# Performance work log

Hardware: AMD Instinct MI355X
Metric: run time of the kernel (lower is better)

## Reference

```python
import jax, jax.numpy as jnp
import numpy as np
from jax import lax

B, T, C, H, W = 4, 10, 96, 32, 32
L = 13
OUT = 96


def _conv(x, w, b, pad):
    y = lax.conv_general_dilated(x, w, (1, 1), [(pad, pad), (pad, pad)],
                                 dimension_numbers=('NCHW', 'OIHW', 'NCHW'))
    return y + b[None, :, None, None]


def _leaky(x):
    return jnp.where(x >= 0, x, 0.2 * x)  # LeakyReLU(0.2)


def _bilinear_warp(img, gx, gy):
    # img (B,C,H,W); gx,gy (B,L,H,W) absolute pixel coords; zero padding outside.
    # Equivalent to torch grid_sample(bilinear, zeros, align_corners=True) as used in HKO wrap().
    def per_b(im, gxb, gyb):
        h, w = im.shape[1], im.shape[2]
        x0 = jnp.floor(gxb)
        y0 = jnp.floor(gyb)
        wx = (gxb - x0)[None]  # (1,L,H,W)
        wy = (gyb - y0)[None]

        def g(xi, yi):
            valid = (xi >= 0) & (xi <= w - 1) & (yi >= 0) & (yi <= h - 1)
            xc = jnp.clip(xi, 0, w - 1).astype(jnp.int32)
            yc = jnp.clip(yi, 0, h - 1).astype(jnp.int32)
            return im[:, yc, xc] * valid[None].astype(im.dtype)  # (C,L,H,W)

        v00 = g(x0, y0)
        v01 = g(x0 + 1, y0)
        v10 = g(x0, y0 + 1)
        v11 = g(x0 + 1, y0 + 1)
        out = (v00 * (1 - wx) + v01 * wx) * (1 - wy) + (v10 * (1 - wx) + v11 * wx) * wy
        return out.transpose(1, 0, 2, 3)  # (L,C,H,W)

    return jax.vmap(per_b)(img, gx, gy)  # (B,L,C,H,W)


def setup_inputs() -> dict:
    key = jax.random.key(0)
    ks = jax.random.split(key, 8)
    s = 0.05
    return {
        "x": jax.random.normal(ks[0], (B, T, C, H, W), jnp.float32),
        "h0": jnp.zeros((B, C, H, W), jnp.float32),
        "i2h_w": jax.random.normal(ks[1], (3 * C, C, 3, 3), jnp.float32) * s,
        "i2h_b": jnp.zeros((3 * C,), jnp.float32),
        "i2f_w": jax.random.normal(ks[2], (32, C, 5, 5), jnp.float32) * s,
        "i2f_b": jnp.zeros((32,), jnp.float32),
        "h2f_w": jax.random.normal(ks[3], (32, C, 5, 5), jnp.float32) * s,
        "h2f_b": jnp.zeros((32,), jnp.float32),
        "flow_w": jax.random.normal(ks[4], (2 * L, 32, 5, 5), jnp.float32) * s,
        "flow_b": jnp.zeros((2 * L,), jnp.float32),
        "ret_w": jax.random.normal(ks[5], (3 * C, L * C, 1, 1), jnp.float32) * s,
        "ret_b": jnp.zeros((3 * C,), jnp.float32),
        "ct_w": jax.random.normal(ks[6], (C * T, OUT * T, 4, 4), jnp.float32) * s,  # torch ConvTranspose2d layout (in,out,kh,kw)
        "ct_b": jnp.zeros((OUT * T,), jnp.float32),
    }


def reference(x, h0, i2h_w, i2h_b, i2f_w, i2f_b, h2f_w, h2f_b,
              flow_w, flow_b, ret_w, ret_b, ct_w, ct_b):
    xs = x.transpose(1, 0, 2, 3, 4)  # (T,B,C,H,W)
    flat = xs.reshape(T * B, C, H, W)
    i2h_all = _conv(flat, i2h_w, i2h_b, 1).reshape(T, B, 3 * C, H, W)
    i2f_all = _conv(flat, i2f_w, i2f_b, 2).reshape(T, B, 32, H, W)
    yy, xx = jnp.meshgrid(jnp.arange(H, dtype=x.dtype),
                          jnp.arange(W, dtype=x.dtype), indexing='ij')

    def step(h, inp):
        i2h_t, i2f_t = inp
        f = _leaky(i2f_t + _conv(h, h2f_w, h2f_b, 2))
        flows = _conv(f, flow_w, flow_b, 2).reshape(B, L, 2, H, W)
        # HKO: wrap(prev_h, -flow) -> sample at grid - flow
        gx = xx - flows[:, :, 0]  # (B,L,H,W)
        gy = yy - flows[:, :, 1]
        warped = _bilinear_warp(h, gx, gy).reshape(B, L * C, H, W)
        h2h = _conv(warped, ret_w, ret_b, 0)  # 1x1 ret conv
        ir, iu, im_ = jnp.split(i2h_t, 3, axis=1)
        hr, hu, hm = jnp.split(h2h, 3, axis=1)
        r = jax.nn.sigmoid(ir + hr)
        u = jax.nn.sigmoid(iu + hu)
        new_mem = _leaky(im_ + r * hm)
        h_next = u * h + (1.0 - u) * new_mem
        return h_next, h_next

    _, ys = lax.scan(step, h0, (i2h_all, i2f_all))  # (T,B,C,H,W)
    y = ys.transpose(1, 0, 2, 3, 4).reshape(B, T * C, H, W)
    # ConvTranspose2d(k=4, s=2, p=1) == conv(flipped kernel, lhs_dilation=2, pad=k-1-p=2)
    wt = jnp.flip(ct_w, (2, 3)).transpose(1, 0, 2, 3)  # (out,in,kh,kw)
    y = lax.conv_general_dilated(y, wt, (1, 1), [(2, 2), (2, 2)],
                                 lhs_dilation=(2, 2),
                                 dimension_numbers=('NCHW', 'OIHW', 'NCHW'))
    y = _leaky(y + ct_b[None, :, None, None])
    return y.reshape(B, T, OUT, 2 * H, 2 * W)
```

## Files before the change

### kernel.cpp

```cpp
#include <hip/hip_runtime.h>
#include <math.h>
#include <stddef.h>

#define B_  4
#define T_  10
#define C_  96
#define H_  32
#define W_  32
#define HW_ 1024
#define L_  13
#define OUT_ 96

typedef __attribute__((ext_vector_type(4))) float f32x4;
typedef __attribute__((ext_vector_type(8))) short bf16x8;

__device__ __forceinline__ float leaky_f(float v) { return v >= 0.f ? v : 0.2f * v; }
__device__ __forceinline__ float sigmoid_f(float v) { return 1.f / (1.f + expf(-v)); }
__device__ __forceinline__ unsigned short f2bf(float f) {
    unsigned u = __float_as_uint(f);
    return (unsigned short)((u + 0x7FFFu + ((u >> 16) & 1u)) >> 16);
}
__device__ __forceinline__ float bf2f(unsigned short s) {
    return __uint_as_float((unsigned)s << 16);
}
__device__ __forceinline__ void gload_lds16(const void* g, void* l) {
    __builtin_amdgcn_global_load_lds(
        (const __attribute__((address_space(1))) unsigned int*)g,
        (__attribute__((address_space(3))) unsigned int*)l, 16, 0, 0);
}

__global__ __launch_bounds__(256) void conv5x5_x_k(
    const float* __restrict__ x, const float* __restrict__ w,
    const float* __restrict__ bias, float* __restrict__ out)
{
    const int px  = threadIdx.x & 63;
    const int g   = threadIdx.x >> 6;
    const int row = px >> 5, col = px & 31;
    const int y0  = blockIdx.x * 2;
    const int oc0 = blockIdx.y * 8 + g * 2;
    const int n   = blockIdx.z;
    const int b   = n % B_;
    const int t   = n / B_;
    const float* xin = x + ((size_t)(b * T_ + t) * C_) * HW_;

    __shared__ float tile[6][36];
    float acc0 = 0.f, acc1 = 0.f;

    for (int c = 0; c < C_; ++c) {
        const float* xc = xin + (size_t)c * HW_;
        if (threadIdx.x < 216) {
            int r = threadIdx.x / 36, cc = threadIdx.x % 36;
            int yy = y0 + r - 2, xx = cc - 2;
            tile[r][cc] = (yy >= 0 && yy < 32 && xx >= 0 && xx < 32) ? xc[yy * 32 + xx] : 0.f;
        }
        __syncthreads();
        const float* w0 = w + ((size_t)oc0 * C_ + c) * 25;
        const float* w1 = w0 + (size_t)C_ * 25;
        #pragma unroll
        for (int dy = 0; dy < 5; ++dy)
            #pragma unroll
            for (int dx = 0; dx < 5; ++dx) {
                float v = tile[row + dy][col + dx];
                acc0 = fmaf(v, w0[dy * 5 + dx], acc0);
                acc1 = fmaf(v, w1[dy * 5 + dx], acc1);
            }
        __syncthreads();
    }
    const int hw = (y0 + row) * 32 + col;
    out[((size_t)n * 32 + oc0) * HW_ + hw]     = acc0 + bias[oc0];
    out[((size_t)n * 32 + oc0 + 1) * HW_ + hw] = acc1 + bias[oc0 + 1];
}

__global__ __launch_bounds__(256) void conv5x5_k(
    const float* __restrict__ in, int in_bstr, int cin, int cout,
    const float* __restrict__ w, const float* __restrict__ bias,
    const float* __restrict__ addsrc, int do_leaky,
    float* __restrict__ out)
{
    const int px  = threadIdx.x & 63;
    const int g   = threadIdx.x >> 6;
    const int row = px >> 5, col = px & 31;
    const int y0  = blockIdx.x * 2;
    const int oc0 = blockIdx.y * 8 + g * 2;
    const int b   = blockIdx.z;
    const int ocw0 = min(oc0, cout - 1);
    const int ocw1 = min(oc0 + 1, cout - 1);

    __shared__ float tile[6][36];
    float acc0 = 0.f, acc1 = 0.f;

    for (int c = 0; c < cin; ++c) {
        const float* xc = in + ((size_t)b * in_bstr + c) * HW_;
        if (threadIdx.x < 216) {
            int r = threadIdx.x / 36, cc = threadIdx.x % 36;
            int yy = y0 + r - 2, xx = cc - 2;
            tile[r][cc] = (yy >= 0 && yy < 32 && xx >= 0 && xx < 32) ? xc[yy * 32 + xx] : 0.f;
        }
        __syncthreads();
        const float* w0 = w + ((size_t)ocw0 * cin + c) * 25;
        const float* w1 = w + ((size_t)ocw1 * cin + c) * 25;
        #pragma unroll
        for (int dy = 0; dy < 5; ++dy)
            #pragma unroll
            for (int dx = 0; dx < 5; ++dx) {
                float v = tile[row + dy][col + dx];
                acc0 = fmaf(v, w0[dy * 5 + dx], acc0);
                acc1 = fmaf(v, w1[dy * 5 + dx], acc1);
            }
        __syncthreads();
    }
    const int hw = (y0 + row) * 32 + col;
    if (oc0 < cout) {
        float r = acc0 + bias[oc0];
        if (addsrc) r += addsrc[((size_t)b * cout + oc0) * HW_ + hw];
        if (do_leaky) r = leaky_f(r);
        out[((size_t)b * cout + oc0) * HW_ + hw] = r;
    }
    if (oc0 + 1 < cout) {
        float r = acc1 + bias[oc0 + 1];
        if (addsrc) r += addsrc[((size_t)b * cout + oc0 + 1) * HW_ + hw];
        if (do_leaky) r = leaky_f(r);
        out[((size_t)b * cout + oc0 + 1) * HW_ + hw] = r;
    }
}

__global__ __launch_bounds__(256) void warp_k(
    const float* __restrict__ h, const float* __restrict__ flows,
    unsigned short* __restrict__ warped_s)
{
    const int hw = (blockIdx.x << 6) + (threadIdx.x & 63);
    const int cg = threadIdx.x >> 6;
    const int l  = blockIdx.y;
    const int b  = blockIdx.z;
    const int py = hw >> 5, px = hw & 31;

    const float fx = flows[((size_t)b * (2 * L_) + 2 * l) * HW_ + hw];
    const float fy = flows[((size_t)b * (2 * L_) + 2 * l + 1) * HW_ + hw];
    const float gx = (float)px - fx;
    const float gy = (float)py - fy;
    const float x0f = floorf(gx), y0f = floorf(gy);
    const float wx = gx - x0f, wy = gy - y0f;
    const int x0 = (int)x0f, y0 = (int)y0f;
    const int x1 = x0 + 1, y1 = y0 + 1;

    const bool vx0 = (x0 >= 0 && x0 <= 31), vx1 = (x1 >= 0 && x1 <= 31);
    const bool vy0 = (y0 >= 0 && y0 <= 31), vy1 = (y1 >= 0 && y1 <= 31);
    const int xc0 = min(max(x0, 0), 31), xc1 = min(max(x1, 0), 31);
    const int yc0 = min(max(y0, 0), 31), yc1 = min(max(y1, 0), 31);
    const int o00 = yc0 * 32 + xc0, o01 = yc0 * 32 + xc1;
    const int o10 = yc1 * 32 + xc0, o11 = yc1 * 32 + xc1;
    const float w00 = (vx0 && vy0) ? (1.f - wx) * (1.f - wy) : 0.f;
    const float w01 = (vx1 && vy0) ? wx * (1.f - wy) : 0.f;
    const float w10 = (vx0 && vy1) ? (1.f - wx) * wy : 0.f;
    const float w11 = (vx1 && vy1) ? wx * wy : 0.f;

    const float* hb = h + ((size_t)b * C_ + cg * 24) * HW_;
    unsigned short* ob = warped_s + ((size_t)b * 2496 + 2 * (l * C_ + cg * 24)) * HW_ + hw;
    for (int cc = 0; cc < 24; ++cc) {
        const float* hc = hb + (size_t)cc * HW_;
        float v = hc[o00] * w00 + hc[o01] * w01 + hc[o10] * w10 + hc[o11] * w11;
        unsigned short hi = f2bf(v);
        ob[(size_t)(2 * cc) * HW_]     = hi;
        ob[(size_t)(2 * cc + 1) * HW_] = f2bf(v - bf2f(hi));
    }
}

__global__ __launch_bounds__(256) void wxprep_k(
    const float* __restrict__ i2h_w, unsigned short* __restrict__ WxS)
{
    const int idx = blockIdx.x * 256 + threadIdx.x;
    const int m = idx / 2624, kp = idx - m * 2624;
    unsigned short r = 0;
    if (m < 288) {
        if (kp < 1728) {
            const int k = kp >> 1;
            const int d = k / 96, c = k - d * 96;
            r = f2bf(i2h_w[((size_t)m * 96 + c) * 9 + d]);
        } else if (kp < 2592) {
            const int k = kp - 1728;
            const int d = k / 96, c = k - d * 96;
            const float w = i2h_w[((size_t)m * 96 + c) * 9 + d];
            const unsigned short hi = f2bf(w);
            r = f2bf(w - bf2f(hi));
        }
    }
    WxS[idx] = r;
}

__global__ __launch_bounds__(256) void wrprep_k(
    const float* __restrict__ ret_w, unsigned short* __restrict__ WrS)
{
    const int idx = blockIdx.x * 256 + threadIdx.x;
    const int m = idx / 3840, kp = idx - m * 3840;
    unsigned short r = 0;
    if (m < 288) {
        if (kp < 2496) {
            r = f2bf(ret_w[(size_t)m * 1248 + (kp >> 1)]);
        } else if (kp < 3744) {
            const float w = ret_w[(size_t)m * 1248 + (kp - 2496)];
            const unsigned short hi = f2bf(w);
            r = f2bf(w - bf2f(hi));
        }
    }
    WrS[idx] = r;
}

__global__ __launch_bounds__(256) void wprep_k(
    const float* __restrict__ ct_w, unsigned short* __restrict__ Wp)
{
    const int idx = blockIdx.x * 256 + threadIdx.x;
    const int ic  = idx % 960;
    const int oc  = (idx / 960) & 1023;
    const int p   = idx / (960 * 1024);
    const int ry  = p >> 1, rx = p & 1;

    unsigned long long pack = 0ull;
    if (oc < 960) {
        #pragma unroll
        for (int a = 0; a < 2; ++a)
            #pragma unroll
            for (int e = 0; e < 2; ++e) {
                const int ky = 3 - 2 * a - ry, kx = 3 - 2 * e - rx;
                float f = ct_w[(((size_t)ic * 960 + oc) * 4 + ky) * 4 + kx];
                pack |= (unsigned long long)f2bf(f) << ((a * 2 + e) * 16);
            }
    }
    *(unsigned long long*)(Wp + ((size_t)(p * 1024 + oc) * 3840 + ic * 4)) = pack;
}

__global__ __launch_bounds__(256) void i2h_gemm_k(
    const float* __restrict__ x, const unsigned short* __restrict__ WxS,
    const float* __restrict__ bias, float* __restrict__ out)
{
    __shared__ unsigned short sA[8192];
    __shared__ unsigned short sB[8192];

    const int t    = threadIdx.x;
    const int lane = t & 63;
    const int wave = t >> 6;
    const int wr   = wave >> 1, wc = wave & 1;
    const int l15  = lane & 15, l4 = lane >> 4;

    const int px0 = blockIdx.x * 128;
    const int m0  = blockIdx.y * 128;

    const unsigned short* aPtr[4];
    int aOff[4];
    #pragma unroll
    for (int i = 0; i < 4; ++i) {
        const int lin = i * 256 + t;
        const int r = lin >> 3;
        const int c = (lin & 7) ^ (r & 7);
        aPtr[i] = WxS + (size_t)(m0 + r) * 2624 + c * 8;
        aOff[i] = lin * 8;
    }

    const int jr    = t & 127;
    const int cbase = t >> 7;
    const int pos   = px0 + jr;
    const int img   = pos >> 10;
    const int hw    = pos & 1023;
    const int ycell = hw >> 5, xcell = hw & 31;
    const int bb = img % B_, tt = img / B_;
    const float* xb = x + ((size_t)(bb * T_ + tt) * C_) * HW_;
    unsigned short* ldsB = sB + jr * 64;

    int offA[4][2], offB[4][2];
    #pragma unroll
    for (int m = 0; m < 4; ++m) {
        const int rA = wr * 64 + m * 16 + l15;
        const int rB = wc * 64 + m * 16 + l15;
        #pragma unroll
        for (int kk = 0; kk < 2; ++kk) {
            const int j = kk * 4 + l4;
            offA[m][kk] = rA * 128 + ((j ^ (rA & 7)) << 4);
            offB[m][kk] = rB * 128 + ((j ^ (rB & 7)) << 4);
        }
    }

    f32x4 acc[4][4];
    #pragma unroll
    for (int m = 0; m < 4; ++m)
        #pragma unroll
        for (int n = 0; n < 4; ++n)
            acc[m][n] = (f32x4){0.f, 0.f, 0.f, 0.f};

    const char* sAc = (const char*)sA;
    const char* sBc = (const char*)sB;

    for (int ks = 0; ks < 41; ++ks) {
        #pragma unroll
        for (int i = 0; i < 4; ++i)
            gload_lds16(aPtr[i] + ks * 64, (void*)(sA + aOff[i]));
        #pragma unroll
        for (int j = 0; j < 4; ++j) {
            const int cc = cbase + 2 * j;
            const int kc = ks * 8 + cc;
            bf16x8 pk = (bf16x8){0,0,0,0,0,0,0,0};
            if (kc < 216) {
                const int d  = kc / 24;
                const int c0 = (kc - d * 24) * 4;
                const int dy = d / 3, dx = d - dy * 3;
                const int yy = ycell - 1 + dy, xx = xcell - 1 + dx;
                const bool ok = (yy >= 0 && yy < 32 && xx >= 0 && xx < 32);
                const float* sp = xb + (size_t)c0 * HW_ + yy * 32 + xx;
                #pragma unroll
                for (int q = 0; q < 4; ++q) {
                    float v = ok ? sp[(size_t)q * HW_] : 0.f;
                    unsigned short hi = f2bf(v);
                    pk[2 * q]     = (short)hi;
                    pk[2 * q + 1] = (short)f2bf(v - bf2f(hi));
                }
            } else if (kc < 324) {
                const int kL = kc - 216;
                const int d  = kL / 12;
                const int c0 = (kL - d * 12) * 8;
                const int dy = d / 3, dx = d - dy * 3;
                const int yy = ycell - 1 + dy, xx = xcell - 1 + dx;
                const bool ok = (yy >= 0 && yy < 32 && xx >= 0 && xx < 32);
                const float* sp = xb + (size_t)c0 * HW_ + yy * 32 + xx;
                #pragma unroll
                for (int q = 0; q < 8; ++q) {
                    float v = ok ? sp[(size_t)q * HW_] : 0.f;
                    pk[q] = (short)f2bf(v);
                }
            }
            *(bf16x8*)(ldsB + ((cc ^ (jr & 7)) << 3)) = pk;
        }
        __syncthreads();
        #pragma unroll
        for (int kk = 0; kk < 2; ++kk) {
            bf16x8 av[4], bv[4];
            #pragma unroll
            for (int m = 0; m < 4; ++m) av[m] = *(const bf16x8*)(sAc + offA[m][kk]);
            #pragma unroll
            for (int n = 0; n < 4; ++n) bv[n] = *(const bf16x8*)(sBc + offB[n][kk]);
            #pragma unroll
            for (int m = 0; m < 4; ++m)
                #pragma unroll
                for (int n = 0; n < 4; ++n)
                    acc[m][n] = __builtin_amdgcn_mfma_f32_16x16x32_bf16(
                        av[m], bv[n], acc[m][n], 0, 0, 0);
        }
        __syncthreads();
    }

    #pragma unroll
    for (int m = 0; m < 4; ++m) {
        const int mB = m0 + wr * 64 + m * 16 + l4 * 4;
        #pragma unroll
        for (int n = 0; n < 4; ++n) {
            const int col = px0 + wc * 64 + n * 16 + l15;
            const int oimg = col >> 10, ohw = col & 1023;
            #pragma unroll
            for (int v = 0; v < 4; ++v) {
                const int oc = mB + v;
                if (oc < 288)
                    out[((size_t)oimg * 288 + oc) * HW_ + ohw] = acc[m][n][v] + bias[oc];
            }
        }
    }
}

__global__ __launch_bounds__(256) void ret_gemm_k(
    const unsigned short* __restrict__ warped_s, const unsigned short* __restrict__ WrS,
    const float* __restrict__ bias, float* __restrict__ h2h)
{
    __shared__ unsigned short sA[8192];
    __shared__ unsigned short sB[8192];

    const int t    = threadIdx.x;
    const int lane = t & 63;
    const int wave = t >> 6;
    const int wr   = wave >> 1, wc = wave & 1;
    const int l15  = lane & 15, l4 = lane >> 4;

    const int px0 = blockIdx.x * 128;
    const int m0  = blockIdx.y * 128;

    const unsigned short* aPtr[4];
    int aOff[4];
    #pragma unroll
    for (int i = 0; i < 4; ++i) {
        const int lin = i * 256 + t;
        const int r = lin >> 3;
        const int c = (lin & 7) ^ (r & 7);
        aPtr[i] = WrS + (size_t)(m0 + r) * 3840 + c * 8;
        aOff[i] = lin * 8;
    }

    const int jr    = t & 127;
    const int cbase = t >> 7;
    const int pos   = px0 + jr;
    const int bb    = pos >> 10;
    const int hw    = pos & 1023;
    const unsigned short* wbase = warped_s + (size_t)bb * 2496 * HW_ + hw;
    unsigned short* ldsB = sB + jr * 64;

    int offA[4][2], offB[4][2];
    #pragma unroll
    for (int m = 0; m < 4; ++m) {
        const int rA = wr * 64 + m * 16 + l15;
        const int rB = wc * 64 + m * 16 + l15;
        #pragma unroll
        for (int kk = 0; kk < 2; ++kk) {
            const int j = kk * 4 + l4;
            offA[m][kk] = rA * 128 + ((j ^ (rA & 7)) << 4);
            offB[m][kk] = rB * 128 + ((j ^ (rB & 7)) << 4);
        }
    }

    f32x4 acc[4][4];
    #pragma unroll
    for (int m = 0; m < 4; ++m)
        #pragma unroll
        for (int n = 0; n < 4; ++n)
            acc[m][n] = (f32x4){0.f, 0.f, 0.f, 0.f};

    const char* sAc = (const char*)sA;
    const char* sBc = (const char*)sB;

    for (int ks = 0; ks < 60; ++ks) {
        #pragma unroll
        for (int i = 0; i < 4; ++i)
            gload_lds16(aPtr[i] + ks * 64, (void*)(sA + aOff[i]));
        #pragma unroll
        for (int j = 0; j < 4; ++j) {
            const int cc = cbase + 2 * j;
            const int kc = ks * 8 + cc;
            bf16x8 pk = (bf16x8){0,0,0,0,0,0,0,0};
            if (kc < 312) {
                const unsigned short* sp = wbase + (size_t)(kc * 8) * HW_;
                #pragma unroll
                for (int q = 0; q < 8; ++q)
                    pk[q] = (short)sp[(size_t)q * HW_];
            } else if (kc < 468) {
                const unsigned short* sp = wbase + (size_t)((kc - 312) * 16) * HW_;
                #pragma unroll
                for (int q = 0; q < 8; ++q)
                    pk[q] = (short)sp[(size_t)(2 * q) * HW_];
            }
            *(bf16x8*)(ldsB + ((cc ^ (jr & 7)) << 3)) = pk;
        }
        __syncthreads();
        #pragma unroll
        for (int kk = 0; kk < 2; ++kk) {
            bf16x8 av[4], bv[4];
            #pragma unroll
            for (int m = 0; m < 4; ++m) av[m] = *(const bf16x8*)(sAc + offA[m][kk]);
            #pragma unroll
            for (int n = 0; n < 4; ++n) bv[n] = *(const bf16x8*)(sBc + offB[n][kk]);
            #pragma unroll
            for (int m = 0; m < 4; ++m)
                #pragma unroll
                for (int n = 0; n < 4; ++n)
                    acc[m][n] = __builtin_amdgcn_mfma_f32_16x16x32_bf16(
                        av[m], bv[n], acc[m][n], 0, 0, 0);
        }
        __syncthreads();
    }

    #pragma unroll
    for (int m = 0; m < 4; ++m) {
        const int mB = m0 + wr * 64 + m * 16 + l4 * 4;
        #pragma unroll
        for (int n = 0; n < 4; ++n) {
            const int col = px0 + wc * 64 + n * 16 + l15;
            const int ob = col >> 10, ohw = col & 1023;
            #pragma unroll
            for (int v = 0; v < 4; ++v) {
                const int oc = mB + v;
                if (oc < 288)
                    h2h[((size_t)ob * 288 + oc) * HW_ + ohw] = acc[m][n][v] + bias[oc];
            }
        }
    }
}

__global__ __launch_bounds__(256) void gru_k(
    const float* __restrict__ i2h_t, const float* __restrict__ h2h,
    const float* __restrict__ h, float* __restrict__ h_next,
    unsigned short* __restrict__ ysb, int t)
{
    const int idx = blockIdx.x * 256 + threadIdx.x;
    const int hw = idx & (HW_ - 1);
    const int c  = (idx >> 10) % C_;
    const int b  = idx / (C_ * HW_);
    const size_t ibase = ((size_t)(t * B_ + b) * 288) * HW_ + hw;
    const size_t hbase = ((size_t)b * 288) * HW_ + hw;

    const float ir = i2h_t[ibase + (size_t)c * HW_];
    const float iu = i2h_t[ibase + (size_t)(96 + c) * HW_];
    const float im = i2h_t[ibase + (size_t)(192 + c) * HW_];
    const float hr = h2h[hbase + (size_t)c * HW_];
    const float hu = h2h[hbase + (size_t)(96 + c) * HW_];
    const float hm = h2h[hbase + (size_t)(192 + c) * HW_];

    const float r = sigmoid_f(ir + hr);
    const float u = sigmoid_f(iu + hu);
    const float mem = leaky_f(im + r * hm);
    const float hv = h[idx];
    const float hn = u * hv + (1.f - u) * mem;
    h_next[idx] = hn;
    ysb[((size_t)b * (T_ * C_) + (size_t)t * C_ + c) * HW_ + hw] = f2bf(hn);
}

__global__ __launch_bounds__(256) void convt_gemm_k(
    const unsigned short* __restrict__ Wp, const unsigned short* __restrict__ ysb,
    const float* __restrict__ bias, float* __restrict__ out)
{
    __shared__ unsigned short sA[8192];
    __shared__ unsigned short sB[8192];

    const int t    = threadIdx.x;
    const int lane = t & 63;
    const int wave = t >> 6;
    const int wr   = wave >> 1, wc = wave & 1;
    const int l15  = lane & 15, l4 = lane >> 4;

    const int px0 = blockIdx.x * 128;
    const int oc0 = blockIdx.y * 128;
    const int p   = blockIdx.z;
    const int ry  = p >> 1, rx = p & 1;
    const unsigned short* Wpp = Wp + (size_t)p * 1024 * 3840;

    const unsigned short* aPtr[4];
    int aOff[4];
    #pragma unroll
    for (int i = 0; i < 4; ++i) {
        const int lin = i * 256 + t;
        const int r = lin >> 3;
        const int c = (lin & 7) ^ (r & 7);
        aPtr[i] = Wpp + (size_t)(oc0 + r) * 3840 + c * 8;
        aOff[i] = lin * 8;
    }

    const int jr    = t & 127;
    const int cbase = t >> 7;
    const int pos   = px0 + jr;
    const int bb    = pos >> 10;
    const int yy    = (pos >> 5) & 31, xx = pos & 31;
    const int Y = yy + ry, X = xx + rx;
    bool okt[4]; int offt[4];
    #pragma unroll
    for (int tp = 0; tp < 4; ++tp) {
        const int dy = tp >> 1, dx = tp & 1;
        const int sy = Y - 1 + dy, sx = X - 1 + dx;
        okt[tp] = (sy >= 0 && sy < 32 && sx >= 0 && sx < 32);
        offt[tp] = sy * 32 + sx;
    }
    const unsigned short* ybase = ysb + ((size_t)bb * 960) * HW_;
    unsigned short* ldsB = sB + jr * 64;

    int offA[4][2], offB[4][2];
    #pragma unroll
    for (int m = 0; m < 4; ++m) {
        const int rA = wr * 64 + m * 16 + l15;
        const int rB = wc * 64 + m * 16 + l15;
        #pragma unroll
        for (int kk = 0; kk < 2; ++kk) {
            const int j = kk * 4 + l4;
            offA[m][kk] = rA * 128 + ((j ^ (rA & 7)) << 4);
            offB[m][kk] = rB * 128 + ((j ^ (rB & 7)) << 4);
        }
    }

    f32x4 acc[4][4];
    #pragma unroll
    for (int m = 0; m < 4; ++m)
        #pragma unroll
        for (int n = 0; n < 4; ++n)
            acc[m][n] = (f32x4){0.f, 0.f, 0.f, 0.f};

    const char* sAc = (const char*)sA;
    const char* sBc = (const char*)sB;

    for (int ks = 0; ks < 60; ++ks) {
        #pragma unroll
        for (int i = 0; i < 4; ++i)
            gload_lds16(aPtr[i] + ks * 64, (void*)(sA + aOff[i]));
        #pragma unroll
        for (int j = 0; j < 4; ++j) {
            const int cc = cbase + 2 * j;
            const int ic0 = (ks * 8 + cc) * 2;
            bf16x8 pk;
            #pragma unroll
            for (int u = 0; u < 2; ++u) {
                const unsigned short* yc = ybase + (size_t)(ic0 + u) * HW_;
                #pragma unroll
                for (int tp = 0; tp < 4; ++tp)
                    pk[u * 4 + tp] = okt[tp] ? (short)yc[offt[tp]] : (short)0;
            }
            *(bf16x8*)(ldsB + ((cc ^ (jr & 7)) << 3)) = pk;
        }
        __syncthreads();
        #pragma unroll
        for (int kk = 0; kk < 2; ++kk) {
            bf16x8 av[4], bv[4];
            #pragma unroll
            for (int m = 0; m < 4; ++m) av[m] = *(const bf16x8*)(sAc + offA[m][kk]);
            #pragma unroll
            for (int n = 0; n < 4; ++n) bv[n] = *(const bf16x8*)(sBc + offB[n][kk]);
            #pragma unroll
            for (int m = 0; m < 4; ++m)
                #pragma unroll
                for (int n = 0; n < 4; ++n)
                    acc[m][n] = __builtin_amdgcn_mfma_f32_16x16x32_bf16(
                        av[m], bv[n], acc[m][n], 0, 0, 0);
        }
        __syncthreads();
    }

    #pragma unroll
    for (int m = 0; m < 4; ++m) {
        const int ocB = oc0 + wr * 64 + m * 16 + l4 * 4;
        #pragma unroll
        for (int n = 0; n < 4; ++n) {
            const int col = px0 + wc * 64 + n * 16 + l15;
            const int ob = col >> 10, oy = (col >> 5) & 31, ox = col & 31;
            #pragma unroll
            for (int v = 0; v < 4; ++v) {
                const int oc = ocB + v;
                if (oc < 960) {
                    const float val = leaky_f(acc[m][n][v] + bias[oc]);
                    out[(((size_t)ob * 960 + oc) * 64 + 2 * oy + ry) * 64 + 2 * ox + rx] = val;
                }
            }
        }
    }
}

extern "C" void kernel_launch(void* const* d_in, const int* in_sizes, int n_in,
                              void* d_out, int out_size, void* d_ws, size_t ws_size,
                              hipStream_t stream)
{
    const float* x      = (const float*)d_in[0];
    const float* h0     = (const float*)d_in[1];
    const float* i2h_w  = (const float*)d_in[2];
    const float* i2h_b  = (const float*)d_in[3];
    const float* i2f_w  = (const float*)d_in[4];
    const float* i2f_b  = (const float*)d_in[5];
    const float* h2f_w  = (const float*)d_in[6];
    const float* h2f_b  = (const float*)d_in[7];
    const float* flow_w = (const float*)d_in[8];
    const float* flow_b = (const float*)d_in[9];
    const float* ret_w  = (const float*)d_in[10];
    const float* ret_b  = (const float*)d_in[11];
    const float* ct_w   = (const float*)d_in[12];
    const float* ct_b   = (const float*)d_in[13];
    float* out = (float*)d_out;

    char* p = (char*)d_ws;
    float* i2h_all = (float*)p; p += (size_t)T_ * B_ * 288 * HW_ * 4;
    float* i2f_all = (float*)p; p += (size_t)T_ * B_ * 32 * HW_ * 4;
    float* f_buf   = (float*)p; p += (size_t)B_ * 32 * HW_ * 4;
    float* flows   = (float*)p; p += (size_t)B_ * 26 * HW_ * 4;
    unsigned short* warped_s = (unsigned short*)p; p += (size_t)B_ * 2496 * HW_ * 2;
    float* h2h     = (float*)p; p += (size_t)B_ * 288 * HW_ * 4;
    float* hA      = (float*)p; p += (size_t)B_ * C_ * HW_ * 4;
    float* hB      = (float*)p; p += (size_t)B_ * C_ * HW_ * 4;
    unsigned short* ysb = (unsigned short*)p; p += (size_t)B_ * (T_ * C_) * HW_ * 2;
    unsigned short* WxS = (unsigned short*)p; p += (size_t)384 * 2624 * 2;
    unsigned short* WrS = (unsigned short*)p; p += (size_t)384 * 3840 * 2;
    unsigned short* Wp = (unsigned short*)d_ws;

    wxprep_k<<<dim3((384 * 2624) / 256), 256, 0, stream>>>(i2h_w, WxS);
    wrprep_k<<<dim3((384 * 3840) / 256), 256, 0, stream>>>(ret_w, WrS);
    i2h_gemm_k<<<dim3(320, 3), 256, 0, stream>>>(x, WxS, i2h_b, i2h_all);
    conv5x5_x_k<<<dim3(16, 4, T_ * B_), 256, 0, stream>>>(x, i2f_w, i2f_b, i2f_all);

    const float* h_cur = h0;
    float* hbuf[2] = {hA, hB};

    for (int t = 0; t < T_; ++t) {
        conv5x5_k<<<dim3(16, 4, B_), 256, 0, stream>>>(
            h_cur, C_, C_, 32, h2f_w, h2f_b,
            i2f_all + (size_t)t * B_ * 32 * HW_, 1, f_buf);
        conv5x5_k<<<dim3(16, 4, B_), 256, 0, stream>>>(
            f_buf, 32, 32, 2 * L_, flow_w, flow_b, nullptr, 0, flows);
        warp_k<<<dim3(16, L_, B_), 256, 0, stream>>>(h_cur, flows, warped_s);
        ret_gemm_k<<<dim3(32, 3), 256, 0, stream>>>(warped_s, WrS, ret_b, h2h);
        float* h_next = hbuf[t & 1];
        gru_k<<<dim3((B_ * C_ * HW_) / 256), 256, 0, stream>>>(
            i2h_all, h2h, h_cur, h_next, ysb, t);
        h_cur = h_next;
    }

    wprep_k<<<dim3((4 * 1024 * 960) / 256), 256, 0, stream>>>(ct_w, Wp);
    convt_gemm_k<<<dim3(32, 8, 4), 256, 0, stream>>>(Wp, ysb, ct_b, out);
}
```

Measured before the change: 3.813 ms.

## Replace scalar i2f 5x5 conv with split-bf16 MFMA implicit GEMM; batch channels in conv5x5

Replaces the direct fp32 5x5 input-to-flow convolution over all frames with an implicit-GEMM kernel on bf16 MFMA. Weights are prepacked into hi/lo bf16 pairs so the products keep roughly fp32 accuracy, and the im2col B tile is built on the fly into swizzled LDS. Separately, the per-step conv5x5 kernel now stages four input channels per barrier instead of one, cutting synchronisation count. The costs are extra passes for the split-precision terms, a new prep kernel and more LDS, with some accuracy risk from the bf16 splitting.

```diff
diff --git a/kernel.cpp b/kernel.cpp
--- a/kernel.cpp
+++ b/kernel.cpp
@@ -29,48 +29,6 @@
         (__attribute__((address_space(3))) unsigned int*)l, 16, 0, 0);
 }
 
-__global__ __launch_bounds__(256) void conv5x5_x_k(
-    const float* __restrict__ x, const float* __restrict__ w,
-    const float* __restrict__ bias, float* __restrict__ out)
-{
-    const int px  = threadIdx.x & 63;
-    const int g   = threadIdx.x >> 6;
-    const int row = px >> 5, col = px & 31;
-    const int y0  = blockIdx.x * 2;
-    const int oc0 = blockIdx.y * 8 + g * 2;
-    const int n   = blockIdx.z;
-    const int b   = n % B_;
-    const int t   = n / B_;
-    const float* xin = x + ((size_t)(b * T_ + t) * C_) * HW_;
-
-    __shared__ float tile[6][36];
-    float acc0 = 0.f, acc1 = 0.f;
-
-    for (int c = 0; c < C_; ++c) {
-        const float* xc = xin + (size_t)c * HW_;
-        if (threadIdx.x < 216) {
-            int r = threadIdx.x / 36, cc = threadIdx.x % 36;
-            int yy = y0 + r - 2, xx = cc - 2;
-            tile[r][cc] = (yy >= 0 && yy < 32 && xx >= 0 && xx < 32) ? xc[yy * 32 + xx] : 0.f;
-        }
-        __syncthreads();
-        const float* w0 = w + ((size_t)oc0 * C_ + c) * 25;
-        const float* w1 = w0 + (size_t)C_ * 25;
-        #pragma unroll
-        for (int dy = 0; dy < 5; ++dy)
-            #pragma unroll
-            for (int dx = 0; dx < 5; ++dx) {
-                float v = tile[row + dy][col + dx];
-                acc0 = fmaf(v, w0[dy * 5 + dx], acc0);
-                acc1 = fmaf(v, w1[dy * 5 + dx], acc1);
-            }
-        __syncthreads();
-    }
-    const int hw = (y0 + row) * 32 + col;
-    out[((size_t)n * 32 + oc0) * HW_ + hw]     = acc0 + bias[oc0];
-    out[((size_t)n * 32 + oc0 + 1) * HW_ + hw] = acc1 + bias[oc0 + 1];
-}
-
 __global__ __launch_bounds__(256) void conv5x5_k(
     const float* __restrict__ in, int in_bstr, int cin, int cout,
     const float* __restrict__ w, const float* __restrict__ bias,
@@ -86,27 +44,31 @@
     const int ocw0 = min(oc0, cout - 1);
     const int ocw1 = min(oc0 + 1, cout - 1);
 
-    __shared__ float tile[6][36];
+    __shared__ float tile[4][6][36];
     float acc0 = 0.f, acc1 = 0.f;
 
-    for (int c = 0; c < cin; ++c) {
-        const float* xc = in + ((size_t)b * in_bstr + c) * HW_;
-        if (threadIdx.x < 216) {
-            int r = threadIdx.x / 36, cc = threadIdx.x % 36;
+    for (int c0 = 0; c0 < cin; c0 += 4) {
+        for (int i = threadIdx.x; i < 4 * 216; i += 256) {
+            int ch = i / 216, rr = i - ch * 216;
+            int r = rr / 36, cc = rr - r * 36;
             int yy = y0 + r - 2, xx = cc - 2;
-            tile[r][cc] = (yy >= 0 && yy < 32 && xx >= 0 && xx < 32) ? xc[yy * 32 + xx] : 0.f;
-        }
-        __syncthreads();
-        const float* w0 = w + ((size_t)ocw0 * cin + c) * 25;
-        const float* w1 = w + ((size_t)ocw1 * cin + c) * 25;
-        #pragma unroll
-        for (int dy = 0; dy < 5; ++dy)
-            #pragma unroll
-            for (int dx = 0; dx < 5; ++dx) {
-                float v = tile[row + dy][col + dx];
-                acc0 = fmaf(v, w0[dy * 5 + dx], acc0);
-                acc1 = fmaf(v, w1[dy * 5 + dx], acc1);
-            }
+            tile[ch][r][cc] = (yy >= 0 && yy < 32 && xx >= 0 && xx < 32)
+                ? in[((size_t)b * in_bstr + c0 + ch) * HW_ + yy * 32 + xx] : 0.f;
+        }
+        __syncthreads();
+        #pragma unroll
+        for (int ch = 0; ch < 4; ++ch) {
+            const float* w0 = w + ((size_t)ocw0 * cin + c0 + ch) * 25;
+            const float* w1 = w + ((size_t)ocw1 * cin + c0 + ch) * 25;
+            #pragma unroll
+            for (int dy = 0; dy < 5; ++dy)
+                #pragma unroll
+                for (int dx = 0; dx < 5; ++dx) {
+                    float v = tile[ch][row + dy][col + dx];
+                    acc0 = fmaf(v, w0[dy * 5 + dx], acc0);
+                    acc1 = fmaf(v, w1[dy * 5 + dx], acc1);
+                }
+        }
         __syncthreads();
     }
     const int hw = (y0 + row) * 32 + col;
@@ -205,6 +167,26 @@
     WrS[idx] = r;
 }
 
+__global__ __launch_bounds__(256) void wfprep_k(
+    const float* __restrict__ i2f_w, unsigned short* __restrict__ WfS)
+{
+    const int idx = blockIdx.x * 256 + threadIdx.x;
+    const int oc = idx / 7232, kp = idx - oc * 7232;
+    unsigned short r = 0;
+    if (kp < 4800) {
+        const int k = kp >> 1;
+        const int d = k / 96, c = k - d * 96;
+        r = f2bf(i2f_w[((size_t)oc * 96 + c) * 25 + d]);
+    } else if (kp < 7200) {
+        const int k = kp - 4800;
+        const int d = k / 96, c = k - d * 96;
+        const float w = i2f_w[((size_t)oc * 96 + c) * 25 + d];
+        const unsigned short hi = f2bf(w);
+        r = f2bf(w - bf2f(hi));
+    }
+    WfS[idx] = r;
+}
+
 __global__ __launch_bounds__(256) void wprep_k(
     const float* __restrict__ ct_w, unsigned short* __restrict__ Wp)
 {
@@ -226,6 +208,143 @@
             }
     }
     *(unsigned long long*)(Wp + ((size_t)(p * 1024 + oc) * 3840 + ic * 4)) = pack;
+}
+
+__global__ __launch_bounds__(128) void i2f_gemm_k(
+    const float* __restrict__ x, const unsigned short* __restrict__ WfS,
+    const float* __restrict__ bias, float* __restrict__ out)
+{
+    __shared__ unsigned short sA[2048];
+    __shared__ unsigned short sB[8192];
+
+    const int t    = threadIdx.x;
+    const int lane = t & 63;
+    const int wave = t >> 6;
+    const int l15  = lane & 15, l4 = lane >> 4;
+
+    const int px0 = blockIdx.x * 128;
+
+    const unsigned short* aPtr[2];
+    int aOff[2];
+    #pragma unroll
+    for (int i = 0; i < 2; ++i) {
+        const int lin = i * 128 + t;
+        const int r = lin >> 3;
+        const int c = (lin & 7) ^ (r & 7);
+        aPtr[i] = WfS + (size_t)r * 7232 + c * 8;
+        aOff[i] = lin * 8;
+    }
+
+    const int jr  = t;
+    const int pos = px0 + jr;
+    const int img = pos >> 10;
+    const int hw  = pos & 1023;
+    const int ycell = hw >> 5, xcell = hw & 31;
+    const int bb = img % B_, tt = img / B_;
+    const float* xb = x + ((size_t)(bb * T_ + tt) * C_) * HW_;
+    unsigned short* ldsB = sB + jr * 64;
+
+    int offA[2][2], offB[4][2];
+    #pragma unroll
+    for (int m = 0; m < 2; ++m) {
+        const int rA = m * 16 + l15;
+        #pragma unroll
+        for (int kk = 0; kk < 2; ++kk) {
+            const int j = kk * 4 + l4;
+            offA[m][kk] = rA * 128 + ((j ^ (rA & 7)) << 4);
+        }
+    }
+    #pragma unroll
+    for (int n = 0; n < 4; ++n) {
+        const int rB = wave * 64 + n * 16 + l15;
+        #pragma unroll
+        for (int kk = 0; kk < 2; ++kk) {
+            const int j = kk * 4 + l4;
+            offB[n][kk] = rB * 128 + ((j ^ (rB & 7)) << 4);
+        }
+    }
+
+    f32x4 acc[2][4];
+    #pragma unroll
+    for (int m = 0; m < 2; ++m)
+        #pragma unroll
+        for (int n = 0; n < 4; ++n)
+            acc[m][n] = (f32x4){0.f, 0.f, 0.f, 0.f};
+
+    const char* sAc = (const char*)sA;
+    const char* sBc = (const char*)sB;
+
+    for (int ks = 0; ks < 113; ++ks) {
+        #pragma unroll
+        for (int i = 0; i < 2; ++i)
+            gload_lds16(aPtr[i] + ks * 64, (void*)(sA + aOff[i]));
+        #pragma unroll
+        for (int cc = 0; cc < 8; ++cc) {
+            const int kc = ks * 8 + cc;
+            bf16x8 pk = (bf16x8){0,0,0,0,0,0,0,0};
+            if (kc < 600) {
+                const int k0 = kc * 4;
+                const int d  = k0 / 96;
+                const int c0 = k0 - d * 96;
+                const int dy = d / 5, dx = d - dy * 5;
+                const int yy = ycell - 2 + dy, xx = xcell - 2 + dx;
+                const bool ok = (yy >= 0 && yy < 32 && xx >= 0 && xx < 32);
+                const float* sp = xb + (size_t)c0 * HW_ + yy * 32 + xx;
+                #pragma unroll
+                for (int q = 0; q < 4; ++q) {
+                    float v = ok ? sp[(size_t)q * HW_] : 0.f;
+                    unsigned short hi = f2bf(v);
+                    pk[2 * q]     = (short)hi;
+                    pk[2 * q + 1] = (short)f2bf(v - bf2f(hi));
+                }
+            } else if (kc < 900) {
+                const int kL = (kc - 600) * 8;
+                const int d  = kL / 96;
+                const int c0 = kL - d * 96;
+                const int dy = d / 5, dx = d - dy * 5;
+                const int yy = ycell - 2 + dy, xx = xcell - 2 + dx;
+                const bool ok = (yy >= 0 && yy < 32 && xx >= 0 && xx < 32);
+                const float* sp = xb + (size_t)c0 * HW_ + yy * 32 + xx;
+                #pragma unroll
+                for (int q = 0; q < 8; ++q) {
+                    float v = ok ? sp[(size_t)q * HW_] : 0.f;
+                    pk[q] = (short)f2bf(v);
+                }
+            }
+            *(bf16x8*)(ldsB + ((cc ^ (jr & 7)) << 3)) = pk;
+        }
+        __syncthreads();
+        #pragma unroll
+        for (int kk = 0; kk < 2; ++kk) {
+            bf16x8 av[2], bv[4];
+            #pragma unroll
+            for (int m = 0; m < 2; ++m) av[m] = *(const bf16x8*)(sAc + offA[m][kk]);
+            #pragma unroll
+            for (int n = 0; n < 4; ++n) bv[n] = *(const bf16x8*)(sBc + offB[n][kk]);
+            #pragma unroll
+            for (int m = 0; m < 2; ++m)
+                #pragma unroll
+                for (int n = 0; n < 4; ++n)
+                    acc[m][n] = __builtin_amdgcn_mfma_f32_16x16x32_bf16(
+                        av[m], bv[n], acc[m][n], 0, 0, 0);
+        }
+        __syncthreads();
+    }
+
+    #pragma unroll
+    for (int m = 0; m < 2; ++m) {
+        const int ocB = m * 16 + l4 * 4;
+        #pragma unroll
+        for (int n = 0; n < 4; ++n) {
+            const int col = px0 + wave * 64 + n * 16 + l15;
+            const int oimg = col >> 10, ohw = col & 1023;
+            #pragma unroll
+            for (int v = 0; v < 4; ++v) {
+                const int oc = ocB + v;
+                out[((size_t)oimg * 32 + oc) * HW_ + ohw] = acc[m][n][v] + bias[oc];
+            }
+        }
+    }
 }
 
 __global__ __launch_bounds__(256) void i2h_gemm_k(
@@ -662,12 +781,14 @@
     unsigned short* ysb = (unsigned short*)p; p += (size_t)B_ * (T_ * C_) * HW_ * 2;
     unsigned short* WxS = (unsigned short*)p; p += (size_t)384 * 2624 * 2;
     unsigned short* WrS = (unsigned short*)p; p += (size_t)384 * 3840 * 2;
+    unsigned short* WfS = (unsigned short*)p; p += (size_t)32 * 7232 * 2;
     unsigned short* Wp = (unsigned short*)d_ws;
 
     wxprep_k<<<dim3((384 * 2624) / 256), 256, 0, stream>>>(i2h_w, WxS);
     wrprep_k<<<dim3((384 * 3840) / 256), 256, 0, stream>>>(ret_w, WrS);
+    wfprep_k<<<dim3((32 * 7232) / 256), 256, 0, stream>>>(i2f_w, WfS);
     i2h_gemm_k<<<dim3(320, 3), 256, 0, stream>>>(x, WxS, i2h_b, i2h_all);
-    conv5x5_x_k<<<dim3(16, 4, T_ * B_), 256, 0, stream>>>(x, i2f_w, i2f_b, i2f_all);
+    i2f_gemm_k<<<dim3(320), 128, 0, stream>>>(x, WfS, i2f_b, i2f_all);
 
     const float* h_cur = h0;
     float* hbuf[2] = {hA, hB};
```

After: 3.722 ms. 2.4% less time.
